# Performance work log

Measured on AMD Instinct MI355X. Metric: run time of the kernel, lower is better.

Reference implementation:

```python
import jax, jax.numpy as jnp
import numpy as np

N = 8192
F_IN = 256
F_OUT = 64
ALPHA = 0.2  # leaky relu negative slope
NEG_BIG = -9e15


def _xavier_uniform(key, shape, gain=1.414):
    fan_in, fan_out = shape[0], shape[1]
    bound = gain * np.sqrt(6.0 / (fan_in + fan_out))
    return jax.random.uniform(key, shape, jnp.float32, -bound, bound)


def setup_inputs() -> dict:
    key = jax.random.key(0)
    k = jax.random.split(key, 6)
    x = jax.random.normal(k[0], (N, F_IN), jnp.float32)
    adj_in = jax.random.randint(k[1], (N, N), 0, 2).astype(jnp.int32)
    adj_out = jax.random.randint(k[2], (N, N), 0, 2).astype(jnp.int32)
    W_in = _xavier_uniform(k[3], (F_IN, F_OUT))
    W_out = _xavier_uniform(k[4], (F_IN, F_OUT))
    a = _xavier_uniform(k[5], (2 * F_OUT, 1))
    return {"x": x, "adj_in": adj_in, "adj_out": adj_out,
            "W_in": W_in, "W_out": W_out, "a": a}


def _gat_branch(h, adj, a):
    # scores: cat([h_i, h_j]) @ a == (h @ a_src)_i + (h @ a_dst)_j
    a_src = a[:F_OUT, 0]   # (F_OUT,)
    a_dst = a[F_OUT:, 0]   # (F_OUT,)
    e = jax.nn.leaky_relu((h @ a_src)[:, None] + (h @ a_dst)[None, :], ALPHA)  # (N, N)
    e = jnp.where(adj > 0, e, jnp.float32(NEG_BIG))
    att = jax.nn.softmax(e, axis=1)
    return att @ h  # (N, F_OUT)


def reference(x, adj_in, adj_out, W_in, W_out, a):
    h_in = x @ W_in
    h_out = x @ W_out
    h_prime_in = _gat_branch(h_in, adj_in, a)
    h_prime_out = _gat_branch(h_out, adj_out, a)
    h_prime = (h_prime_in + h_prime_out) * 0.5
    return jax.nn.elu(h_prime)  # concat=True path
```

## Files before the change

kernel.cpp:

```cpp
#include <hip/hip_runtime.h>
#include <hip/hip_bf16.h>
#include <stdint.h>


#define NN 8192
#define ALPHA 0.2f
#define L2E 1.44269504088896f
#define AL2E 0.288539008177792f

typedef _Float16 f16;
typedef _Float16 f16x2 __attribute__((ext_vector_type(2)));
typedef _Float16 f16x4 __attribute__((ext_vector_type(4)));
typedef _Float16 f16x8 __attribute__((ext_vector_type(8)));
typedef float f32x4 __attribute__((ext_vector_type(4)));
typedef unsigned int u32;

#define WS_WT    0u
#define WS_E1    0u
#define WS_E2    32768u
#define WS_HT    65536u
#define WS_SRC   2162688u
#define WS_DST   2228224u
#define WS_DMAX  2293760u
#define WS_PACC  2294016u

static __device__ __forceinline__ void gload16(const void* g, void* l) {
    __builtin_amdgcn_global_load_lds(
        (const __attribute__((address_space(1))) void*)g,
        (__attribute__((address_space(3))) void*)l, 16, 0, 0);
}

__global__ __launch_bounds__(256) void k1_wt(const float* __restrict__ Win,
                                             const float* __restrict__ Wout,
                                             f16* __restrict__ WT) {
    int c = blockIdx.x;
    int k = threadIdx.x;
    const float* W = (c < 64) ? Win : Wout;
    int cc = c & 63;
    WT[(size_t)c * 256 + k] = (f16)W[(size_t)k * 64 + cc];
}

__global__ __launch_bounds__(64) void k2_h(const float* __restrict__ x,
                                           const f16* __restrict__ WT,
                                           const float* __restrict__ a,
                                           f16* __restrict__ HT,
                                           float* __restrict__ srcw,
                                           float* __restrict__ dstw) {
    int l = threadIdx.x;
    int l15 = l & 15, lhi = l >> 4;
    int row0 = blockIdx.x * 16;

    f32x4 acc[8];
#pragma unroll
    for (int n = 0; n < 8; n++) { acc[n][0]=0.f; acc[n][1]=0.f; acc[n][2]=0.f; acc[n][3]=0.f; }

#pragma unroll
    for (int kc = 0; kc < 8; kc++) {
        int k = kc * 32 + lhi * 8;
        const float* xp = x + (size_t)(row0 + l15) * 256 + k;
        float4 xa = *(const float4*)xp;
        float4 xb = *(const float4*)(xp + 4);
        f16x8 af;
        af[0]=(f16)xa.x; af[1]=(f16)xa.y; af[2]=(f16)xa.z; af[3]=(f16)xa.w;
        af[4]=(f16)xb.x; af[5]=(f16)xb.y; af[6]=(f16)xb.z; af[7]=(f16)xb.w;
#pragma unroll
        for (int n = 0; n < 8; n++) {
            f16x8 bf = *(const f16x8*)(WT + (size_t)(16 * n + l15) * 256 + k);
            acc[n] = __builtin_amdgcn_mfma_f32_16x16x32_f16(af, bf, acc[n], 0, 0, 0);
        }
    }

    float as4[4], ad4[4];
#pragma unroll
    for (int nn = 0; nn < 4; nn++) {
        as4[nn] = a[16 * nn + l15];
        ad4[nn] = a[64 + 16 * nn + l15];
    }

    float s_in[4] = {0,0,0,0}, d_in[4] = {0,0,0,0};
    float s_out[4] = {0,0,0,0}, d_out[4] = {0,0,0,0};

#pragma unroll
    for (int n = 0; n < 8; n++) {
        int b = n >> 2;
        int ci = 16 * (n & 3) + l15;
        int jj = row0 + 4 * lhi;
        f16x4 hv;
#pragma unroll
        for (int q = 0; q < 4; q++) hv[q] = (f16)acc[n][q];
        *(f16x4*)(HT + (size_t)b * 524288 + (size_t)(jj >> 3) * 512 + (size_t)ci * 8 + (jj & 7)) = hv;
#pragma unroll
        for (int q = 0; q < 4; q++) {
            float v = acc[n][q];
            if (b == 0) { s_in[q]  += v * as4[n & 3]; d_in[q]  += v * ad4[n & 3]; }
            else        { s_out[q] += v * as4[n & 3]; d_out[q] += v * ad4[n & 3]; }
        }
    }

#pragma unroll
    for (int q = 0; q < 4; q++) {
#pragma unroll
        for (int m = 1; m < 16; m <<= 1) {
            s_in[q]  += __shfl_xor(s_in[q],  m, 64);
            d_in[q]  += __shfl_xor(d_in[q],  m, 64);
            s_out[q] += __shfl_xor(s_out[q], m, 64);
            d_out[q] += __shfl_xor(d_out[q], m, 64);
        }
    }
    if (l15 == 0) {
        int row = row0 + 4 * lhi;
#pragma unroll
        for (int q = 0; q < 4; q++) {
            srcw[row + q]        = s_in[q];
            srcw[8192 + row + q] = s_out[q];
            dstw[row + q]        = d_in[q];
            dstw[8192 + row + q] = d_out[q];
        }
    }
}

__global__ __launch_bounds__(256) void k3_dmax(const float* __restrict__ dstw,
                                               float* __restrict__ dmax) {
    __shared__ float red[2][4];
    int t = threadIdx.x;
    int l = t & 63, w = t >> 6;
    for (int b = 0; b < 2; b++) {
        float v = -1e30f;
        for (int i = t; i < 8192; i += 256) v = fmaxf(v, dstw[b * 8192 + i]);
#pragma unroll
        for (int m = 1; m < 64; m <<= 1) v = fmaxf(v, __shfl_xor(v, m, 64));
        if (l == 0) red[b][w] = v;
    }
    __syncthreads();
    if (t == 0) dmax[0] = fmaxf(fmaxf(red[0][0], red[0][1]), fmaxf(red[0][2], red[0][3]));
    if (t == 1) dmax[1] = fmaxf(fmaxf(red[1][0], red[1][1]), fmaxf(red[1][2], red[1][3]));
}

__global__ __launch_bounds__(256) void k3b_e(const float* __restrict__ dstw,
                                             const float* __restrict__ dmax,
                                             f16* __restrict__ E1,
                                             f16* __restrict__ E2) {
    int i = blockIdx.x * 256 + threadIdx.x;
    int b = i >> 13;
    float d = dstw[i] - dmax[b];
    E1[i] = (f16)exp2f(d * L2E);
    E2[i] = (f16)exp2f(d * AL2E);
}

__global__ __launch_bounds__(256, 4) void k4_main(const int* __restrict__ adj_in,
                                                  const int* __restrict__ adj_out,
                                                  const f16* __restrict__ HT,
                                                  const float* __restrict__ srcw,
                                                  const float* __restrict__ dmaxp,
                                                  const f16* __restrict__ E1g,
                                                  const f16* __restrict__ E2g,
                                                  float* __restrict__ pacc) {
    __shared__ __align__(16) char lds[33024];

    int t = threadIdx.x;
    int branch = blockIdx.x & 1;
    int row0 = (blockIdx.x >> 1) * 16;
    const int* adj = (branch ? adj_out : adj_in) + (size_t)row0 * NN;
    const f16* htg = HT + (size_t)branch * (64 * NN);
    const f16* e1b = E1g + branch * NN;
    const f16* e2b = E2g + branch * NN;

    int l = t & 63, wv = t >> 6;
    int l15 = l & 15, lhi = l >> 4;
    int sw = l15 & 7;

    float srcv = srcw[branch * NN + row0 + l15];
    float dmaxv = dmaxp[branch];
    float md = srcv + dmaxv;
    float mlog = fmaxf(md, ALPHA * md) * L2E;
    f16 k1h = (f16)exp2f(md * L2E - mlog);
    f16 k2h = (f16)exp2f(ALPHA * md * L2E - mlog);
    f16x8 k1v, k2v;
#pragma unroll
    for (int i = 0; i < 8; i++) { k1v[i] = k1h; k2v[i] = k2h; }

    f32x4 acc[4];
#pragma unroll
    for (int n = 0; n < 4; n++) { acc[n][0]=0.f; acc[n][1]=0.f; acc[n][2]=0.f; acc[n][3]=0.f; }
    float dn = 0.f;
    f16x2 one2; one2[0] = (f16)1.f; one2[1] = (f16)1.f;

    auto stage = [&](int tile, int buf) {
        const int* base = adj + tile * 256;
#pragma unroll
        for (int i = 0; i < 4; i++) {
            int r = wv * 4 + i;
            const int* src = base + (size_t)r * NN + ((l ^ (r & 7)) << 2);
            gload16(src, lds + buf * 16384 + r * 1024);
        }
    };

    stage(0, 0);
    asm volatile("s_waitcnt vmcnt(0)" ::: "memory");
    __builtin_amdgcn_s_barrier();

    for (int tile = 0; tile < 32; tile++) {
        int buf = tile & 1;
        if (tile < 31) stage(tile + 1, buf ^ 1);

#pragma unroll
        for (int ss = 0; ss < 2; ss++) {
            int jloc = wv * 64 + ss * 32;
            int qb = (jloc >> 2) + 2 * lhi;
            const char* rowp = lds + buf * 16384 + l15 * 1024;
            int4 a0 = *(const int4*)(rowp + (((qb    ) ^ sw) << 4));
            int4 a1 = *(const int4*)(rowp + (((qb + 1) ^ sw) << 4));

            int jg = tile * 256 + jloc + lhi * 8;
            f16x8 e1v = *(const f16x8*)(e1b + jg);
            f16x8 e2v = *(const f16x8*)(e2b + jg);
            f16x8 w = __builtin_elementwise_max(e1v * k1v, e2v * k2v);

            union { u32 u[4]; f16x8 h; } mu;
            mu.u[0] = (u32)(a0.x + (a0.y << 16)) * 0x3C00u;
            mu.u[1] = (u32)(a0.z + (a0.w << 16)) * 0x3C00u;
            mu.u[2] = (u32)(a1.x + (a1.y << 16)) * 0x3C00u;
            mu.u[3] = (u32)(a1.z + (a1.w << 16)) * 0x3C00u;
            w = w * mu.h;

            union { f16x8 h; f16x2 p[4]; } wu; wu.h = w;
#if __has_builtin(__builtin_amdgcn_fdot2)
            dn = __builtin_amdgcn_fdot2(wu.p[0], one2, dn, false);
            dn = __builtin_amdgcn_fdot2(wu.p[1], one2, dn, false);
            dn = __builtin_amdgcn_fdot2(wu.p[2], one2, dn, false);
            dn = __builtin_amdgcn_fdot2(wu.p[3], one2, dn, false);
#else
#pragma unroll
            for (int e = 0; e < 8; e++) dn += (float)w[e];
#endif

            const f16* hb = htg + (size_t)(jg >> 3) * 512 + l15 * 8;
            f16x8 b0 = *(const f16x8*)(hb);
            f16x8 b1 = *(const f16x8*)(hb + 128);
            f16x8 b2 = *(const f16x8*)(hb + 256);
            f16x8 b3 = *(const f16x8*)(hb + 384);
            acc[0] = __builtin_amdgcn_mfma_f32_16x16x32_f16(w, b0, acc[0], 0, 0, 0);
            acc[1] = __builtin_amdgcn_mfma_f32_16x16x32_f16(w, b1, acc[1], 0, 0, 0);
            acc[2] = __builtin_amdgcn_mfma_f32_16x16x32_f16(w, b2, acc[2], 0, 0, 0);
            acc[3] = __builtin_amdgcn_mfma_f32_16x16x32_f16(w, b3, acc[3], 0, 0, 0);
        }

        asm volatile("s_waitcnt vmcnt(0)" ::: "memory");
        __builtin_amdgcn_s_barrier();
    }

    dn += __shfl_xor(dn, 16, 64);
    dn += __shfl_xor(dn, 32, 64);

    float* accL = (float*)lds;
    float* dnp  = (float*)(lds + 16384);
    float* dnr  = (float*)(lds + 16384 + 256);
    if (lhi == 0) dnp[wv * 16 + l15] = dn;
#pragma unroll
    for (int n = 0; n < 4; n++)
#pragma unroll
        for (int q = 0; q < 4; q++)
            accL[wv * 1024 + (4 * lhi + q) * 64 + 16 * n + l15] = acc[n][q];
    __syncthreads();

    if (t < 16) dnr[t] = 1.0f / (dnp[t] + dnp[16 + t] + dnp[32 + t] + dnp[48 + t]);
    __syncthreads();

    int r = t >> 4;
    int c4 = (t & 15) * 4;
    float inv = dnr[r];
    float4 o;
    o.x = (accL[r*64+c4+0] + accL[1024+r*64+c4+0] + accL[2048+r*64+c4+0] + accL[3072+r*64+c4+0]) * inv;
    o.y = (accL[r*64+c4+1] + accL[1024+r*64+c4+1] + accL[2048+r*64+c4+1] + accL[3072+r*64+c4+1]) * inv;
    o.z = (accL[r*64+c4+2] + accL[1024+r*64+c4+2] + accL[2048+r*64+c4+2] + accL[3072+r*64+c4+2]) * inv;
    o.w = (accL[r*64+c4+3] + accL[1024+r*64+c4+3] + accL[2048+r*64+c4+3] + accL[3072+r*64+c4+3]) * inv;
    *(float4*)(pacc + (size_t)branch * 524288 + (size_t)(row0 + r) * 64 + c4) = o;
}

__global__ __launch_bounds__(256) void k5_combine(const float* __restrict__ pacc,
                                                  float* __restrict__ out) {
    size_t idx = (size_t)blockIdx.x * 256 + threadIdx.x;
    float4 p0 = *(const float4*)(pacc + idx * 4);
    float4 p1 = *(const float4*)(pacc + 524288 + idx * 4);
    float4 o;
    float v;
    v = 0.5f * (p0.x + p1.x); o.x = (v > 0.f) ? v : (exp2f(v * L2E) - 1.f);
    v = 0.5f * (p0.y + p1.y); o.y = (v > 0.f) ? v : (exp2f(v * L2E) - 1.f);
    v = 0.5f * (p0.z + p1.z); o.z = (v > 0.f) ? v : (exp2f(v * L2E) - 1.f);
    v = 0.5f * (p0.w + p1.w); o.w = (v > 0.f) ? v : (exp2f(v * L2E) - 1.f);
    *(float4*)(out + idx * 4) = o;
}

extern "C" void kernel_launch(void* const* d_in, const int* in_sizes, int n_in,
                              void* d_out, int out_size, void* d_ws, size_t ws_size,
                              hipStream_t stream) {
    const float* x       = (const float*)d_in[0];
    const int*   adj_in  = (const int*)d_in[1];
    const int*   adj_out = (const int*)d_in[2];
    const float* W_in    = (const float*)d_in[3];
    const float* W_out   = (const float*)d_in[4];
    const float* a       = (const float*)d_in[5];
    float* out = (float*)d_out;

    char* ws = (char*)d_ws;
    f16*   WT   = (f16*)(ws + WS_WT);
    f16*   E1   = (f16*)(ws + WS_E1);
    f16*   E2   = (f16*)(ws + WS_E2);
    f16*   HT   = (f16*)(ws + WS_HT);
    float* srcw = (float*)(ws + WS_SRC);
    float* dstw = (float*)(ws + WS_DST);
    float* dmax = (float*)(ws + WS_DMAX);
    float* pacc = (float*)(ws + WS_PACC);

    hipLaunchKernelGGL(k1_wt,     dim3(128),  dim3(256), 0, stream, W_in, W_out, WT);
    hipLaunchKernelGGL(k2_h,      dim3(512),  dim3(64),  0, stream, x, WT, a, HT, srcw, dstw);
    hipLaunchKernelGGL(k3_dmax,   dim3(1),    dim3(256), 0, stream, dstw, dmax);
    hipLaunchKernelGGL(k3b_e,     dim3(64),   dim3(256), 0, stream, dstw, dmax, E1, E2);
    hipLaunchKernelGGL(k4_main,   dim3(1024), dim3(256), 0, stream, adj_in, adj_out, HT, srcw, dmax, E1, E2, pacc);
    hipLaunchKernelGGL(k5_combine,dim3(512),  dim3(256), 0, stream, pacc, out);
}
```

Before: 160.7 us.

## Pack adjacency into bitmasks and fuse both branches with combine

Adds a pre-pass that compresses both int32 adjacency matrices into 1-bit masks. A new main kernel then computes both branches for 32 rows per block, reading masks from LDS, and applies the average plus ELU directly, so the separate combine kernel goes away. The path runs only when the workspace is large enough, otherwise the old path is used. The pack pass still reads the full 512 MB of adjacency, so any gain depends on the new main kernel and the fusion, and it adds an extra 16 MB write and read.

Result: slower. 220.1 us (+37.0%).

```diff
diff --git a/kernel.cpp b/kernel.cpp
--- a/kernel.cpp
+++ b/kernel.cpp
@@ -23,6 +23,8 @@
 #define WS_DST   2228224u
 #define WS_DMAX  2293760u
 #define WS_PACC  2294016u
+#define WS_BITS  2294016u
+#define WS_BIG_NEED 19071232ull
 
 static __device__ __forceinline__ void gload16(const void* g, void* l) {
     __builtin_amdgcn_global_load_lds(
@@ -145,6 +147,176 @@
     float d = dstw[i] - dmax[b];
     E1[i] = (f16)exp2f(d * L2E);
     E2[i] = (f16)exp2f(d * AL2E);
+}
+
+__global__ __launch_bounds__(256) void k_pack(const int* __restrict__ adj_in,
+                                              const int* __restrict__ adj_out,
+                                              u32* __restrict__ bits) {
+    int t = threadIdx.x;
+    int l = t & 63, wv = t >> 6;
+    int nwaves = gridDim.x * 4;
+    for (int c = blockIdx.x * 4 + wv; c < 524288; c += nwaves) {
+        int branch = c >> 18;
+        int row = (c >> 5) & 8191;
+        int ch = c & 31;
+        const int* src = (branch ? adj_out : adj_in) + (size_t)row * 8192 + ch * 256 + l * 4;
+        int4 a = *(const int4*)src;
+        u32 nib = (u32)(a.x > 0) | ((u32)(a.y > 0) << 1) | ((u32)(a.z > 0) << 2) | ((u32)(a.w > 0) << 3);
+        u32 v = nib << ((l & 7) * 4);
+        v |= (u32)__shfl_xor((int)v, 1, 64);
+        v |= (u32)__shfl_xor((int)v, 2, 64);
+        v |= (u32)__shfl_xor((int)v, 4, 64);
+        if ((l & 7) == 0)
+            bits[(size_t)branch * 2097152 + (size_t)row * 256 + ch * 8 + (l >> 3)] = v;
+    }
+}
+
+__global__ __launch_bounds__(512, 2) void k4_bits(const u32* __restrict__ bitsg,
+                                                  const f16* __restrict__ HT,
+                                                  const float* __restrict__ srcw,
+                                                  const float* __restrict__ dmaxp,
+                                                  const f16* __restrict__ E1g,
+                                                  const f16* __restrict__ E2g,
+                                                  float* __restrict__ out) {
+    __shared__ __align__(16) char lds[66560];
+
+    int t = threadIdx.x;
+    int row0 = blockIdx.x * 32;
+    int l = t & 63, wv = t >> 6;
+    int B = wv >> 2, q = wv & 3;
+    int l15 = l & 15, lhi = l >> 4;
+    int lhi8 = lhi * 8;
+
+#pragma unroll
+    for (int p = 0; p < 8; p++) {
+        int idx = p * 512 + t;
+        int bb = idx >> 11;
+        int r  = (idx >> 6) & 31;
+        int c16 = idx & 63;
+        uint4 v = *(const uint4*)(bitsg + (size_t)bb * 2097152 + (size_t)(row0 + r) * 256 + c16 * 4);
+        *(uint4*)(lds + bb * 33280 + r * 1040 + c16 * 16) = v;
+    }
+
+    const float* srcb = srcw + B * NN;
+    float dmaxv = dmaxp[B];
+    f16x8 k1v0, k2v0, k1v1, k2v1;
+    {
+        float srcv = srcb[row0 + l15];
+        float md = srcv + dmaxv;
+        float mlog = fmaxf(md, ALPHA * md) * L2E;
+        f16 k1 = (f16)exp2f(md * L2E - mlog);
+        f16 k2 = (f16)exp2f(ALPHA * md * L2E - mlog);
+#pragma unroll
+        for (int i = 0; i < 8; i++) { k1v0[i] = k1; k2v0[i] = k2; }
+    }
+    {
+        float srcv = srcb[row0 + 16 + l15];
+        float md = srcv + dmaxv;
+        float mlog = fmaxf(md, ALPHA * md) * L2E;
+        f16 k1 = (f16)exp2f(md * L2E - mlog);
+        f16 k2 = (f16)exp2f(ALPHA * md * L2E - mlog);
+#pragma unroll
+        for (int i = 0; i < 8; i++) { k1v1[i] = k1; k2v1[i] = k2; }
+    }
+
+    const f16* htg = HT + (size_t)B * (64 * NN);
+    const f16* e1b = E1g + B * NN;
+    const f16* e2b = E2g + B * NN;
+    const u32* bl0 = (const u32*)(lds + B * 33280 + l15 * 1040);
+    const u32* bl1 = (const u32*)(lds + B * 33280 + (l15 + 16) * 1040);
+
+    f32x4 acc0[4], acc1[4];
+#pragma unroll
+    for (int n = 0; n < 4; n++) {
+        acc0[n][0]=0.f; acc0[n][1]=0.f; acc0[n][2]=0.f; acc0[n][3]=0.f;
+        acc1[n][0]=0.f; acc1[n][1]=0.f; acc1[n][2]=0.f; acc1[n][3]=0.f;
+    }
+    float dn0 = 0.f, dn1 = 0.f;
+    f16x2 one2; one2[0] = (f16)1.f; one2[1] = (f16)1.f;
+
+    __syncthreads();
+
+    for (int tile = 0; tile < 32; tile++) {
+#pragma unroll
+        for (int ss = 0; ss < 2; ss++) {
+            int widx = tile * 8 + q * 2 + ss;
+            u32 bw0 = bl0[widx];
+            u32 bw1 = bl1[widx];
+            int jg = tile * 256 + q * 64 + ss * 32 + lhi8;
+
+            f16x8 e1v = *(const f16x8*)(e1b + jg);
+            f16x8 e2v = *(const f16x8*)(e2b + jg);
+
+            u32 by0 = (bw0 >> lhi8) & 0xFFu;
+            u32 by1 = (bw1 >> lhi8) & 0xFFu;
+            union { u32 u[4]; f16x8 h; } m0, m1;
+#pragma unroll
+            for (int p = 0; p < 4; p++) {
+                m0.u[p] = (((by0 >> (2 * p)) & 1u) | (((by0 >> (2 * p + 1)) & 1u) << 16)) * 0x3C00u;
+                m1.u[p] = (((by1 >> (2 * p)) & 1u) | (((by1 >> (2 * p + 1)) & 1u) << 16)) * 0x3C00u;
+            }
+            f16x8 w0 = __builtin_elementwise_max(e1v * k1v0, e2v * k2v0) * m0.h;
+            f16x8 w1 = __builtin_elementwise_max(e1v * k1v1, e2v * k2v1) * m1.h;
+
+            union { f16x8 h; f16x2 pr[4]; } u0, u1;
+            u0.h = w0; u1.h = w1;
+#if __has_builtin(__builtin_amdgcn_fdot2)
+#pragma unroll
+            for (int p = 0; p < 4; p++) {
+                dn0 = __builtin_amdgcn_fdot2(u0.pr[p], one2, dn0, false);
+                dn1 = __builtin_amdgcn_fdot2(u1.pr[p], one2, dn1, false);
+            }
+#else
+#pragma unroll
+            for (int e = 0; e < 8; e++) { dn0 += (float)w0[e]; dn1 += (float)w1[e]; }
+#endif
+
+            const f16* hb = htg + (size_t)(jg >> 3) * 512 + l15 * 8;
+            f16x8 b0 = *(const f16x8*)(hb);
+            f16x8 b1 = *(const f16x8*)(hb + 128);
+            f16x8 b2 = *(const f16x8*)(hb + 256);
+            f16x8 b3 = *(const f16x8*)(hb + 384);
+            acc0[0] = __builtin_amdgcn_mfma_f32_16x16x32_f16(w0, b0, acc0[0], 0, 0, 0);
+            acc0[1] = __builtin_amdgcn_mfma_f32_16x16x32_f16(w0, b1, acc0[1], 0, 0, 0);
+            acc0[2] = __builtin_amdgcn_mfma_f32_16x16x32_f16(w0, b2, acc0[2], 0, 0, 0);
+            acc0[3] = __builtin_amdgcn_mfma_f32_16x16x32_f16(w0, b3, acc0[3], 0, 0, 0);
+            acc1[0] = __builtin_amdgcn_mfma_f32_16x16x32_f16(w1, b0, acc1[0], 0, 0, 0);
+            acc1[1] = __builtin_amdgcn_mfma_f32_16x16x32_f16(w1, b1, acc1[1], 0, 0, 0);
+            acc1[2] = __builtin_amdgcn_mfma_f32_16x16x32_f16(w1, b2, acc1[2], 0, 0, 0);
+            acc1[3] = __builtin_amdgcn_mfma_f32_16x16x32_f16(w1, b3, acc1[3], 0, 0, 0);
+        }
+    }
+
+    dn0 += __shfl_xor(dn0, 16, 64); dn0 += __shfl_xor(dn0, 32, 64);
+    dn1 += __shfl_xor(dn1, 16, 64); dn1 += __shfl_xor(dn1, 32, 64);
+
+    __syncthreads();
+    float* accL = (float*)lds;
+    float* dnp  = (float*)(lds + 65536);
+    if (lhi == 0) { dnp[wv * 32 + l15] = dn0; dnp[wv * 32 + 16 + l15] = dn1; }
+#pragma unroll
+    for (int n = 0; n < 4; n++)
+#pragma unroll
+        for (int qr = 0; qr < 4; qr++) {
+            accL[wv * 2048 + (4 * lhi + qr) * 64 + 16 * n + l15]        = acc0[n][qr];
+            accL[wv * 2048 + (16 + 4 * lhi + qr) * 64 + 16 * n + l15]   = acc1[n][qr];
+        }
+    __syncthreads();
+
+    int r = t >> 4;
+    int c4 = (t & 15) * 4;
+    float inv0 = 1.0f / (dnp[r] + dnp[32 + r] + dnp[64 + r] + dnp[96 + r]);
+    float inv1 = 1.0f / (dnp[128 + r] + dnp[160 + r] + dnp[192 + r] + dnp[224 + r]);
+    float4 o;
+#pragma unroll
+    for (int cc = 0; cc < 4; cc++) {
+        int idx = r * 64 + c4 + cc;
+        float v0 = (accL[idx] + accL[2048 + idx] + accL[4096 + idx] + accL[6144 + idx]) * inv0;
+        float v1 = (accL[8192 + idx] + accL[10240 + idx] + accL[12288 + idx] + accL[14336 + idx]) * inv1;
+        float h = 0.5f * (v0 + v1);
+        ((float*)&o)[cc] = (h > 0.f) ? h : (exp2f(h * L2E) - 1.f);
+    }
+    *(float4*)(out + (size_t)(row0 + r) * 64 + c4) = o;
 }
 
 __global__ __launch_bounds__(256, 4) void k4_main(const int* __restrict__ adj_in,
@@ -310,12 +482,19 @@
     float* srcw = (float*)(ws + WS_SRC);
     float* dstw = (float*)(ws + WS_DST);
     float* dmax = (float*)(ws + WS_DMAX);
-    float* pacc = (float*)(ws + WS_PACC);
-
-    hipLaunchKernelGGL(k1_wt,     dim3(128),  dim3(256), 0, stream, W_in, W_out, WT);
-    hipLaunchKernelGGL(k2_h,      dim3(512),  dim3(64),  0, stream, x, WT, a, HT, srcw, dstw);
-    hipLaunchKernelGGL(k3_dmax,   dim3(1),    dim3(256), 0, stream, dstw, dmax);
-    hipLaunchKernelGGL(k3b_e,     dim3(64),   dim3(256), 0, stream, dstw, dmax, E1, E2);
-    hipLaunchKernelGGL(k4_main,   dim3(1024), dim3(256), 0, stream, adj_in, adj_out, HT, srcw, dmax, E1, E2, pacc);
-    hipLaunchKernelGGL(k5_combine,dim3(512),  dim3(256), 0, stream, pacc, out);
-}
+
+    hipLaunchKernelGGL(k1_wt,   dim3(128), dim3(256), 0, stream, W_in, W_out, WT);
+    hipLaunchKernelGGL(k2_h,    dim3(512), dim3(64),  0, stream, x, WT, a, HT, srcw, dstw);
+    hipLaunchKernelGGL(k3_dmax, dim3(1),   dim3(256), 0, stream, dstw, dmax);
+    hipLaunchKernelGGL(k3b_e,   dim3(64),  dim3(256), 0, stream, dstw, dmax, E1, E2);
+
+    if (ws_size >= WS_BIG_NEED) {
+        u32* bits = (u32*)(ws + WS_BITS);
+        hipLaunchKernelGGL(k_pack,  dim3(2048), dim3(256), 0, stream, adj_in, adj_out, bits);
+        hipLaunchKernelGGL(k4_bits, dim3(256),  dim3(512), 0, stream, bits, HT, srcw, dmax, E1, E2, out);
+    } else {
+        float* pacc = (float*)(ws + WS_PACC);
+        hipLaunchKernelGGL(k4_main,   dim3(1024), dim3(256), 0, stream, adj_in, adj_out, HT, srcw, dmax, E1, E2, pacc);
+        hipLaunchKernelGGL(k5_combine,dim3(512),  dim3(256), 0, stream, pacc, out);
+    }
+}
```

## Deepen adjacency prefetch to a four-buffer ring and hoist per-tile global loads

Applied to the files above, without the earlier changes.

The adjacency staging moves from a double buffer to a four-slot LDS ring. Tiles are now prefetched two iterations ahead, and the full vmcnt(0) wait at the end of each tile is dropped, leaving only a barrier. All E1/E2 and HT global loads for both 32-column sub-steps are issued at the start of the tile, before the next stage, with sched_barriers fencing the order. The goal is more memory latency in flight and less time stalled waiting on each tile's loads. In exchange, LDS doubles and launch bounds drop to 2 blocks per CU, which lowers occupancy. Correctness now depends on the compiler's implicit vmcnt waits on the hoisted loads also retiring the earlier async stage loads.

New measurement: 153.3 us (median of 2 runs). 4.6% less time.

```diff
diff --git a/kernel.cpp b/kernel.cpp
--- a/kernel.cpp
+++ b/kernel.cpp
@@ -147,7 +147,7 @@
     E2[i] = (f16)exp2f(d * AL2E);
 }
 
-__global__ __launch_bounds__(256, 4) void k4_main(const int* __restrict__ adj_in,
+__global__ __launch_bounds__(256, 2) void k4_main(const int* __restrict__ adj_in,
                                                   const int* __restrict__ adj_out,
                                                   const f16* __restrict__ HT,
                                                   const float* __restrict__ srcw,
@@ -155,7 +155,7 @@
                                                   const f16* __restrict__ E1g,
                                                   const f16* __restrict__ E2g,
                                                   float* __restrict__ pacc) {
-    __shared__ __align__(16) char lds[33024];
+    __shared__ __align__(16) char lds[66048];
 
     int t = threadIdx.x;
     int branch = blockIdx.x & 1;
@@ -185,7 +185,8 @@
     float dn = 0.f;
     f16x2 one2; one2[0] = (f16)1.f; one2[1] = (f16)1.f;
 
-    auto stage = [&](int tile, int buf) {
+    auto stage = [&](int tile) {
+        int buf = tile & 3;
         const int* base = adj + tile * 256;
 #pragma unroll
         for (int i = 0; i < 4; i++) {
@@ -195,34 +196,51 @@
         }
     };
 
-    stage(0, 0);
-    asm volatile("s_waitcnt vmcnt(0)" ::: "memory");
+    stage(0);
+    stage(1);
+    asm volatile("s_waitcnt vmcnt(4)");
+    __builtin_amdgcn_sched_barrier(0);
     __builtin_amdgcn_s_barrier();
 
     for (int tile = 0; tile < 32; tile++) {
-        int buf = tile & 1;
-        if (tile < 31) stage(tile + 1, buf ^ 1);
-
-#pragma unroll
-        for (int ss = 0; ss < 2; ss++) {
-            int jloc = wv * 64 + ss * 32;
-            int qb = (jloc >> 2) + 2 * lhi;
-            const char* rowp = lds + buf * 16384 + l15 * 1024;
-            int4 a0 = *(const int4*)(rowp + (((qb    ) ^ sw) << 4));
-            int4 a1 = *(const int4*)(rowp + (((qb + 1) ^ sw) << 4));
-
-            int jg = tile * 256 + jloc + lhi * 8;
-            f16x8 e1v = *(const f16x8*)(e1b + jg);
-            f16x8 e2v = *(const f16x8*)(e2b + jg);
-            f16x8 w = __builtin_elementwise_max(e1v * k1v, e2v * k2v);
-
+        int buf = tile & 3;
+        const char* rowp = lds + buf * 16384 + l15 * 1024;
+
+        int qb0 = (wv * 64 >> 2) + 2 * lhi;
+        int4 a0 = *(const int4*)(rowp + (((qb0    ) ^ sw) << 4));
+        int4 a1 = *(const int4*)(rowp + (((qb0 + 1) ^ sw) << 4));
+        int qb1 = qb0 + 8;
+        int4 a2 = *(const int4*)(rowp + (((qb1    ) ^ sw) << 4));
+        int4 a3 = *(const int4*)(rowp + (((qb1 + 1) ^ sw) << 4));
+
+        int jg0 = tile * 256 + wv * 64 + lhi * 8;
+        int jg1 = jg0 + 32;
+        f16x8 e1v0 = *(const f16x8*)(e1b + jg0);
+        f16x8 e2v0 = *(const f16x8*)(e2b + jg0);
+        f16x8 e1v1 = *(const f16x8*)(e1b + jg1);
+        f16x8 e2v1 = *(const f16x8*)(e2b + jg1);
+        const f16* hb0 = htg + (size_t)(jg0 >> 3) * 512 + l15 * 8;
+        const f16* hb1 = htg + (size_t)(jg1 >> 3) * 512 + l15 * 8;
+        f16x8 b00 = *(const f16x8*)(hb0);
+        f16x8 b01 = *(const f16x8*)(hb0 + 128);
+        f16x8 b02 = *(const f16x8*)(hb0 + 256);
+        f16x8 b03 = *(const f16x8*)(hb0 + 384);
+        f16x8 b10 = *(const f16x8*)(hb1);
+        f16x8 b11 = *(const f16x8*)(hb1 + 128);
+        f16x8 b12 = *(const f16x8*)(hb1 + 256);
+        f16x8 b13 = *(const f16x8*)(hb1 + 384);
+        __builtin_amdgcn_sched_barrier(0);
+
+        if (tile < 30) stage(tile + 2);
+        __builtin_amdgcn_sched_barrier(0);
+
+        {
             union { u32 u[4]; f16x8 h; } mu;
             mu.u[0] = (u32)(a0.x + (a0.y << 16)) * 0x3C00u;
             mu.u[1] = (u32)(a0.z + (a0.w << 16)) * 0x3C00u;
             mu.u[2] = (u32)(a1.x + (a1.y << 16)) * 0x3C00u;
             mu.u[3] = (u32)(a1.z + (a1.w << 16)) * 0x3C00u;
-            w = w * mu.h;
-
+            f16x8 w = __builtin_elementwise_max(e1v0 * k1v, e2v0 * k2v) * mu.h;
             union { f16x8 h; f16x2 p[4]; } wu; wu.h = w;
 #if __has_builtin(__builtin_amdgcn_fdot2)
             dn = __builtin_amdgcn_fdot2(wu.p[0], one2, dn, false);
@@ -233,24 +251,40 @@
 #pragma unroll
             for (int e = 0; e < 8; e++) dn += (float)w[e];
 #endif
-
-            const f16* hb = htg + (size_t)(jg >> 3) * 512 + l15 * 8;
-            f16x8 b0 = *(const f16x8*)(hb);
-            f16x8 b1 = *(const f16x8*)(hb + 128);
-            f16x8 b2 = *(const f16x8*)(hb + 256);
-            f16x8 b3 = *(const f16x8*)(hb + 384);
-            acc[0] = __builtin_amdgcn_mfma_f32_16x16x32_f16(w, b0, acc[0], 0, 0, 0);
-            acc[1] = __builtin_amdgcn_mfma_f32_16x16x32_f16(w, b1, acc[1], 0, 0, 0);
-            acc[2] = __builtin_amdgcn_mfma_f32_16x16x32_f16(w, b2, acc[2], 0, 0, 0);
-            acc[3] = __builtin_amdgcn_mfma_f32_16x16x32_f16(w, b3, acc[3], 0, 0, 0);
-        }
-
-        asm volatile("s_waitcnt vmcnt(0)" ::: "memory");
+            acc[0] = __builtin_amdgcn_mfma_f32_16x16x32_f16(w, b00, acc[0], 0, 0, 0);
+            acc[1] = __builtin_amdgcn_mfma_f32_16x16x32_f16(w, b01, acc[1], 0, 0, 0);
+            acc[2] = __builtin_amdgcn_mfma_f32_16x16x32_f16(w, b02, acc[2], 0, 0, 0);
+            acc[3] = __builtin_amdgcn_mfma_f32_16x16x32_f16(w, b03, acc[3], 0, 0, 0);
+        }
+        {
+            union { u32 u[4]; f16x8 h; } mu;
+            mu.u[0] = (u32)(a2.x + (a2.y << 16)) * 0x3C00u;
+            mu.u[1] = (u32)(a2.z + (a2.w << 16)) * 0x3C00u;
+            mu.u[2] = (u32)(a3.x + (a3.y << 16)) * 0x3C00u;
+            mu.u[3] = (u32)(a3.z + (a3.w << 16)) * 0x3C00u;
+            f16x8 w = __builtin_elementwise_max(e1v1 * k1v, e2v1 * k2v) * mu.h;
+            union { f16x8 h; f16x2 p[4]; } wu; wu.h = w;
+#if __has_builtin(__builtin_amdgcn_fdot2)
+            dn = __builtin_amdgcn_fdot2(wu.p[0], one2, dn, false);
+            dn = __builtin_amdgcn_fdot2(wu.p[1], one2, dn, false);
+            dn = __builtin_amdgcn_fdot2(wu.p[2], one2, dn, false);
+            dn = __builtin_amdgcn_fdot2(wu.p[3], one2, dn, false);
+#else
+#pragma unroll
+            for (int e = 0; e < 8; e++) dn += (float)w[e];
+#endif
+            acc[0] = __builtin_amdgcn_mfma_f32_16x16x32_f16(w, b10, acc[0], 0, 0, 0);
+            acc[1] = __builtin_amdgcn_mfma_f32_16x16x32_f16(w, b11, acc[1], 0, 0, 0);
+            acc[2] = __builtin_amdgcn_mfma_f32_16x16x32_f16(w, b12, acc[2], 0, 0, 0);
+            acc[3] = __builtin_amdgcn_mfma_f32_16x16x32_f16(w, b13, acc[3], 0, 0, 0);
+        }
+
         __builtin_amdgcn_s_barrier();
     }
 
     dn += __shfl_xor(dn, 16, 64);
     dn += __shfl_xor(dn, 32, 64);
+    __syncthreads();
 
     float* accL = (float*)lds;
     float* dnp  = (float*)(lds + 16384);
```

## Process 32 rows per block with 8 waves and triple-buffered adjacency staging

Applied to the files above, without the earlier changes.

The main attention kernel now handles 32 adjacency rows per 512-thread block, so each wave reuses the loaded E1/E2 and HT fragments for two 16-row MFMA groups. It also moves from a double-buffered to a triple-buffered LDS pipeline with a two-tile prefetch distance and partial vmcnt waits, and marks the adjacency loads non-temporal. The intent is to halve the reloads of H and exponent vectors per adjacency byte and keep more streaming loads in flight. In exchange it uses 96KB of LDS per block and doubles the accumulator registers, which lowers the number of resident blocks per CU.

After: 160.9 us. About the same (+0.1%).

```diff
diff --git a/kernel.cpp b/kernel.cpp
--- a/kernel.cpp
+++ b/kernel.cpp
@@ -24,10 +24,10 @@
 #define WS_DMAX  2293760u
 #define WS_PACC  2294016u
 
-static __device__ __forceinline__ void gload16(const void* g, void* l) {
+static __device__ __forceinline__ void gload16_nt(const void* g, void* l) {
     __builtin_amdgcn_global_load_lds(
         (const __attribute__((address_space(1))) void*)g,
-        (__attribute__((address_space(3))) void*)l, 16, 0, 0);
+        (__attribute__((address_space(3))) void*)l, 16, 0, 2);
 }
 
 __global__ __launch_bounds__(256) void k1_wt(const float* __restrict__ Win,
@@ -147,7 +147,7 @@
     E2[i] = (f16)exp2f(d * AL2E);
 }
 
-__global__ __launch_bounds__(256, 4) void k4_main(const int* __restrict__ adj_in,
+__global__ __launch_bounds__(512, 2) void k4_main(const int* __restrict__ adj_in,
                                                   const int* __restrict__ adj_out,
                                                   const f16* __restrict__ HT,
                                                   const float* __restrict__ srcw,
@@ -155,11 +155,11 @@
                                                   const f16* __restrict__ E1g,
                                                   const f16* __restrict__ E2g,
                                                   float* __restrict__ pacc) {
-    __shared__ __align__(16) char lds[33024];
+    __shared__ __align__(16) char lds[98304];
 
     int t = threadIdx.x;
     int branch = blockIdx.x & 1;
-    int row0 = (blockIdx.x >> 1) * 16;
+    int row0 = (blockIdx.x >> 1) * 32;
     const int* adj = (branch ? adj_out : adj_in) + (size_t)row0 * NN;
     const f16* htg = HT + (size_t)branch * (64 * NN);
     const f16* e1b = E1g + branch * NN;
@@ -169,20 +169,34 @@
     int l15 = l & 15, lhi = l >> 4;
     int sw = l15 & 7;
 
-    float srcv = srcw[branch * NN + row0 + l15];
     float dmaxv = dmaxp[branch];
-    float md = srcv + dmaxv;
-    float mlog = fmaxf(md, ALPHA * md) * L2E;
-    f16 k1h = (f16)exp2f(md * L2E - mlog);
-    f16 k2h = (f16)exp2f(ALPHA * md * L2E - mlog);
-    f16x8 k1v, k2v;
-#pragma unroll
-    for (int i = 0; i < 8; i++) { k1v[i] = k1h; k2v[i] = k2h; }
-
-    f32x4 acc[4];
-#pragma unroll
-    for (int n = 0; n < 4; n++) { acc[n][0]=0.f; acc[n][1]=0.f; acc[n][2]=0.f; acc[n][3]=0.f; }
-    float dn = 0.f;
+    f16x8 k1v0, k2v0, k1v1, k2v1;
+    {
+        float srcv = srcw[branch * NN + row0 + l15];
+        float md = srcv + dmaxv;
+        float mlog = fmaxf(md, ALPHA * md) * L2E;
+        f16 k1 = (f16)exp2f(md * L2E - mlog);
+        f16 k2 = (f16)exp2f(ALPHA * md * L2E - mlog);
+#pragma unroll
+        for (int i = 0; i < 8; i++) { k1v0[i] = k1; k2v0[i] = k2; }
+    }
+    {
+        float srcv = srcw[branch * NN + row0 + 16 + l15];
+        float md = srcv + dmaxv;
+        float mlog = fmaxf(md, ALPHA * md) * L2E;
+        f16 k1 = (f16)exp2f(md * L2E - mlog);
+        f16 k2 = (f16)exp2f(ALPHA * md * L2E - mlog);
+#pragma unroll
+        for (int i = 0; i < 8; i++) { k1v1[i] = k1; k2v1[i] = k2; }
+    }
+
+    f32x4 acc0[4], acc1[4];
+#pragma unroll
+    for (int n = 0; n < 4; n++) {
+        acc0[n][0]=0.f; acc0[n][1]=0.f; acc0[n][2]=0.f; acc0[n][3]=0.f;
+        acc1[n][0]=0.f; acc1[n][1]=0.f; acc1[n][2]=0.f; acc1[n][3]=0.f;
+    }
+    float dn0 = 0.f, dn1 = 0.f;
     f16x2 one2; one2[0] = (f16)1.f; one2[1] = (f16)1.f;
 
     auto stage = [&](int tile, int buf) {
@@ -191,89 +205,126 @@
         for (int i = 0; i < 4; i++) {
             int r = wv * 4 + i;
             const int* src = base + (size_t)r * NN + ((l ^ (r & 7)) << 2);
-            gload16(src, lds + buf * 16384 + r * 1024);
+            gload16_nt(src, lds + buf * 32768 + r * 1024);
         }
     };
 
     stage(0, 0);
-    asm volatile("s_waitcnt vmcnt(0)" ::: "memory");
+    stage(1, 1);
+    asm volatile("s_waitcnt vmcnt(4)");
+    __builtin_amdgcn_sched_barrier(0);
     __builtin_amdgcn_s_barrier();
 
+    int js = wv * 32;
+    int qb = (js >> 2) + 2 * lhi;
+
     for (int tile = 0; tile < 32; tile++) {
-        int buf = tile & 1;
-        if (tile < 31) stage(tile + 1, buf ^ 1);
-
-#pragma unroll
-        for (int ss = 0; ss < 2; ss++) {
-            int jloc = wv * 64 + ss * 32;
-            int qb = (jloc >> 2) + 2 * lhi;
-            const char* rowp = lds + buf * 16384 + l15 * 1024;
-            int4 a0 = *(const int4*)(rowp + (((qb    ) ^ sw) << 4));
-            int4 a1 = *(const int4*)(rowp + (((qb + 1) ^ sw) << 4));
-
-            int jg = tile * 256 + jloc + lhi * 8;
-            f16x8 e1v = *(const f16x8*)(e1b + jg);
-            f16x8 e2v = *(const f16x8*)(e2b + jg);
-            f16x8 w = __builtin_elementwise_max(e1v * k1v, e2v * k2v);
-
+        int buf = tile - (tile / 3) * 3;
+        int nbuf = (buf == 2) ? 0 : buf + 1;
+        int nnbuf = (nbuf == 2) ? 0 : nbuf + 1;
+        (void)nbuf;
+
+        int jg = tile * 256 + js + lhi * 8;
+        f16x8 e1v = *(const f16x8*)(e1b + jg);
+        f16x8 e2v = *(const f16x8*)(e2b + jg);
+        const f16* hb = htg + (size_t)(jg >> 3) * 512 + l15 * 8;
+        f16x8 b0 = *(const f16x8*)(hb);
+        f16x8 b1 = *(const f16x8*)(hb + 128);
+        f16x8 b2 = *(const f16x8*)(hb + 256);
+        f16x8 b3 = *(const f16x8*)(hb + 384);
+        __builtin_amdgcn_sched_barrier(0);
+
+        if (tile < 30) stage(tile + 2, nnbuf);
+        __builtin_amdgcn_sched_barrier(0);
+
+        const char* rowp0 = lds + buf * 32768 + l15 * 1024;
+        const char* rowp1 = lds + buf * 32768 + (l15 + 16) * 1024;
+        int4 a0 = *(const int4*)(rowp0 + (((qb    ) ^ sw) << 4));
+        int4 a1 = *(const int4*)(rowp0 + (((qb + 1) ^ sw) << 4));
+        int4 a2 = *(const int4*)(rowp1 + (((qb    ) ^ sw) << 4));
+        int4 a3 = *(const int4*)(rowp1 + (((qb + 1) ^ sw) << 4));
+
+        {
             union { u32 u[4]; f16x8 h; } mu;
             mu.u[0] = (u32)(a0.x + (a0.y << 16)) * 0x3C00u;
             mu.u[1] = (u32)(a0.z + (a0.w << 16)) * 0x3C00u;
             mu.u[2] = (u32)(a1.x + (a1.y << 16)) * 0x3C00u;
             mu.u[3] = (u32)(a1.z + (a1.w << 16)) * 0x3C00u;
-            w = w * mu.h;
-
+            f16x8 w = __builtin_elementwise_max(e1v * k1v0, e2v * k2v0) * mu.h;
             union { f16x8 h; f16x2 p[4]; } wu; wu.h = w;
 #if __has_builtin(__builtin_amdgcn_fdot2)
-            dn = __builtin_amdgcn_fdot2(wu.p[0], one2, dn, false);
-            dn = __builtin_amdgcn_fdot2(wu.p[1], one2, dn, false);
-            dn = __builtin_amdgcn_fdot2(wu.p[2], one2, dn, false);
-            dn = __builtin_amdgcn_fdot2(wu.p[3], one2, dn, false);
+            dn0 = __builtin_amdgcn_fdot2(wu.p[0], one2, dn0, false);
+            dn0 = __builtin_amdgcn_fdot2(wu.p[1], one2, dn0, false);
+            dn0 = __builtin_amdgcn_fdot2(wu.p[2], one2, dn0, false);
+            dn0 = __builtin_amdgcn_fdot2(wu.p[3], one2, dn0, false);
 #else
 #pragma unroll
-            for (int e = 0; e < 8; e++) dn += (float)w[e];
+            for (int e = 0; e < 8; e++) dn0 += (float)w[e];
 #endif
-
-            const f16* hb = htg + (size_t)(jg >> 3) * 512 + l15 * 8;
-            f16x8 b0 = *(const f16x8*)(hb);
-            f16x8 b1 = *(const f16x8*)(hb + 128);
-            f16x8 b2 = *(const f16x8*)(hb + 256);
-            f16x8 b3 = *(const f16x8*)(hb + 384);
-            acc[0] = __builtin_amdgcn_mfma_f32_16x16x32_f16(w, b0, acc[0], 0, 0, 0);
-            acc[1] = __builtin_amdgcn_mfma_f32_16x16x32_f16(w, b1, acc[1], 0, 0, 0);
-            acc[2] = __builtin_amdgcn_mfma_f32_16x16x32_f16(w, b2, acc[2], 0, 0, 0);
-            acc[3] = __builtin_amdgcn_mfma_f32_16x16x32_f16(w, b3, acc[3], 0, 0, 0);
-        }
-
-        asm volatile("s_waitcnt vmcnt(0)" ::: "memory");
+            acc0[0] = __builtin_amdgcn_mfma_f32_16x16x32_f16(w, b0, acc0[0], 0, 0, 0);
+            acc0[1] = __builtin_amdgcn_mfma_f32_16x16x32_f16(w, b1, acc0[1], 0, 0, 0);
+            acc0[2] = __builtin_amdgcn_mfma_f32_16x16x32_f16(w, b2, acc0[2], 0, 0, 0);
+            acc0[3] = __builtin_amdgcn_mfma_f32_16x16x32_f16(w, b3, acc0[3], 0, 0, 0);
+        }
+        {
+            union { u32 u[4]; f16x8 h; } mu;
+            mu.u[0] = (u32)(a2.x + (a2.y << 16)) * 0x3C00u;
+            mu.u[1] = (u32)(a2.z + (a2.w << 16)) * 0x3C00u;
+            mu.u[2] = (u32)(a3.x + (a3.y << 16)) * 0x3C00u;
+            mu.u[3] = (u32)(a3.z + (a3.w << 16)) * 0x3C00u;
+            f16x8 w = __builtin_elementwise_max(e1v * k1v1, e2v * k2v1) * mu.h;
+            union { f16x8 h; f16x2 p[4]; } wu; wu.h = w;
+#if __has_builtin(__builtin_amdgcn_fdot2)
+            dn1 = __builtin_amdgcn_fdot2(wu.p[0], one2, dn1, false);
+            dn1 = __builtin_amdgcn_fdot2(wu.p[1], one2, dn1, false);
+            dn1 = __builtin_amdgcn_fdot2(wu.p[2], one2, dn1, false);
+            dn1 = __builtin_amdgcn_fdot2(wu.p[3], one2, dn1, false);
+#else
+#pragma unroll
+            for (int e = 0; e < 8; e++) dn1 += (float)w[e];
+#endif
+            acc1[0] = __builtin_amdgcn_mfma_f32_16x16x32_f16(w, b0, acc1[0], 0, 0, 0);
+            acc1[1] = __builtin_amdgcn_mfma_f32_16x16x32_f16(w, b1, acc1[1], 0, 0, 0);
+            acc1[2] = __builtin_amdgcn_mfma_f32_16x16x32_f16(w, b2, acc1[2], 0, 0, 0);
+            acc1[3] = __builtin_amdgcn_mfma_f32_16x16x32_f16(w, b3, acc1[3], 0, 0, 0);
+        }
+
+        asm volatile("s_waitcnt vmcnt(4)");
+        __builtin_amdgcn_sched_barrier(0);
         __builtin_amdgcn_s_barrier();
     }
 
-    dn += __shfl_xor(dn, 16, 64);
-    dn += __shfl_xor(dn, 32, 64);
+    dn0 += __shfl_xor(dn0, 16, 64); dn0 += __shfl_xor(dn0, 32, 64);
+    dn1 += __shfl_xor(dn1, 16, 64); dn1 += __shfl_xor(dn1, 32, 64);
+    __syncthreads();
 
     float* accL = (float*)lds;
-    float* dnp  = (float*)(lds + 16384);
-    float* dnr  = (float*)(lds + 16384 + 256);
-    if (lhi == 0) dnp[wv * 16 + l15] = dn;
+    float* dnp  = (float*)(lds + 65536);
+    if (lhi == 0) { dnp[wv * 32 + l15] = dn0; dnp[wv * 32 + 16 + l15] = dn1; }
 #pragma unroll
     for (int n = 0; n < 4; n++)
 #pragma unroll
-        for (int q = 0; q < 4; q++)
-            accL[wv * 1024 + (4 * lhi + q) * 64 + 16 * n + l15] = acc[n][q];
-    __syncthreads();
-
-    if (t < 16) dnr[t] = 1.0f / (dnp[t] + dnp[16 + t] + dnp[32 + t] + dnp[48 + t]);
+        for (int q = 0; q < 4; q++) {
+            accL[wv * 2048 + (4 * lhi + q) * 64 + 16 * n + l15]      = acc0[n][q];
+            accL[wv * 2048 + (16 + 4 * lhi + q) * 64 + 16 * n + l15] = acc1[n][q];
+        }
     __syncthreads();
 
     int r = t >> 4;
     int c4 = (t & 15) * 4;
-    float inv = dnr[r];
+    float dsum = 0.f;
+#pragma unroll
+    for (int w8 = 0; w8 < 8; w8++) dsum += dnp[w8 * 32 + r];
+    float inv = 1.0f / dsum;
     float4 o;
-    o.x = (accL[r*64+c4+0] + accL[1024+r*64+c4+0] + accL[2048+r*64+c4+0] + accL[3072+r*64+c4+0]) * inv;
-    o.y = (accL[r*64+c4+1] + accL[1024+r*64+c4+1] + accL[2048+r*64+c4+1] + accL[3072+r*64+c4+1]) * inv;
-    o.z = (accL[r*64+c4+2] + accL[1024+r*64+c4+2] + accL[2048+r*64+c4+2] + accL[3072+r*64+c4+2]) * inv;
-    o.w = (accL[r*64+c4+3] + accL[1024+r*64+c4+3] + accL[2048+r*64+c4+3] + accL[3072+r*64+c4+3]) * inv;
+#pragma unroll
+    for (int cc = 0; cc < 4; cc++) {
+        int idx = r * 64 + c4 + cc;
+        float s = 0.f;
+#pragma unroll
+        for (int w8 = 0; w8 < 8; w8++) s += accL[w8 * 2048 + idx];
+        ((float*)&o)[cc] = s * inv;
+    }
     *(float4*)(pacc + (size_t)branch * 524288 + (size_t)(row0 + r) * 64 + c4) = o;
 }
 
@@ -316,6 +367,6 @@
     hipLaunchKernelGGL(k2_h,      dim3(512),  dim3(64),  0, stream, x, WT, a, HT, srcw, dstw);
     hipLaunchKernelGGL(k3_dmax,   dim3(1),    dim3(256), 0, stream, dstw, dmax);
     hipLaunchKernelGGL(k3b_e,     dim3(64),   dim3(256), 0, stream, dstw, dmax, E1, E2);
-    hipLaunchKernelGGL(k4_main,   dim3(1024), dim3(256), 0, stream, adj_in, adj_out, HT, srcw, dmax, E1, E2, pacc);
+    hipLaunchKernelGGL(k4_main,   dim3(512),  dim3(512), 0, stream, adj_in, adj_out, HT, srcw, dmax, E1, E2, pacc);
     hipLaunchKernelGGL(k5_combine,dim3(512),  dim3(256), 0, stream, pacc, out);
 }
```
